# Kernel tuning notes

Measured on AMD Instinct MI355X. Metric: run time of the kernel, lower is better.

The kernel has to match this reference:

```python
import jax, jax.numpy as jnp
import numpy as np

B, U, NBS, S = 128, 4, 64, 408
EM_WEIGHT = 0.01  # config['loss']['em_property_weight']


def setup_inputs() -> dict:
    key = jax.random.key(0)
    ks = jax.random.split(key, 11)
    return {
        "atten_re": jax.random.normal(ks[0], (B, U, S), jnp.float32),
        "atten_im": jax.random.normal(ks[1], (B, U, S), jnp.float32),
        "rad_re": jax.random.normal(ks[2], (B, U, NBS, S), jnp.float32),
        "rad_im": jax.random.normal(ks[3], (B, U, NBS, S), jnp.float32),
        "tgt_re": jax.random.normal(ks[4], (B, U, NBS, S), jnp.float32),
        "tgt_im": jax.random.normal(ks[5], (B, U, NBS, S), jnp.float32),
        "weights": jax.random.uniform(ks[6], (S,), jnp.float32),
        "positions": jax.random.normal(ks[7], (B, 3), jnp.float32),
        "ue_positions": jax.random.normal(ks[8], (B, 3), jnp.float32),
        "view_directions": jax.random.normal(ks[9], (B, 3), jnp.float32),
        "bs_antenna_ids": jax.random.randint(ks[10], (B,), 0, NBS, jnp.int64),
    }


def reference(atten_re, atten_im, rad_re, rad_im, tgt_re, tgt_im, weights,
              positions, ue_positions, view_directions, bs_antenna_ids):
    # Vectorized form of the triple loop: the ray-tracer stub contributes
    # nothing; accumulated signal = attenuation * radiation (complex mul),
    # with attenuation broadcast over the BS-antenna axis.
    ar = atten_re[:, :, None, :]  # [B,U,1,S]
    ai = atten_im[:, :, None, :]
    pred_re = ar * rad_re - ai * rad_im  # [B,U,NBS,S]
    pred_im = ar * rad_im + ai * rad_re
    # MSE on real + imag parts, weighted per subcarrier, summed.
    se = (pred_re - tgt_re) ** 2 + (pred_im - tgt_im) ** 2
    received_loss = jnp.sum(se * weights[None, None, None, :])
    # EM property regularization (torch.abs on complex -> magnitude).
    atten_mag = jnp.sqrt(atten_re ** 2 + atten_im ** 2)
    rad_mag = jnp.sqrt(rad_re ** 2 + rad_im ** 2)
    em_loss = (jnp.mean(jax.nn.relu(atten_mag - 1.0) ** 2)
               + jnp.mean(jax.nn.relu(rad_mag - 10.0) ** 2))
    return received_loss + EM_WEIGHT * em_loss
```

## Files before the change

### kernel.cpp

```cpp
#include <hip/hip_runtime.h>

constexpr int kB   = 128;
constexpr int kU   = 4;
constexpr int kNBS = 64;
constexpr int kS   = 408;
constexpr int kS4  = kS / 4;
constexpr unsigned kNQ = (unsigned)kB * kU * kNBS * kS4;
constexpr unsigned kThreads = kNQ / 4;
constexpr unsigned kRowStep = 8192;
constexpr float kEmW     = 0.01f;
constexpr float kInvNRad = 1.0f / ((float)kB * kU * kNBS * kS);
constexpr float kInvNAtt = 1.0f / ((float)kB * kU * kS);

typedef float vfloat4 __attribute__((ext_vector_type(4)));

__global__ void __launch_bounds__(256)
prism_loss_kernel(const vfloat4* __restrict__ atten_re,
                  const vfloat4* __restrict__ atten_im,
                  const vfloat4* __restrict__ rad_re,
                  const vfloat4* __restrict__ rad_im,
                  const vfloat4* __restrict__ tgt_re,
                  const vfloat4* __restrict__ tgt_im,
                  const vfloat4* __restrict__ weights,
                  float* __restrict__ out)
{
    const unsigned tid  = blockIdx.x * 256 + threadIdx.x;
    const unsigned row0 = tid / 102u;
    const unsigned s4   = tid - row0 * 102u;
    const unsigned abase = (row0 >> 6) * 102u + s4;
    const bool do_att = ((row0 & 63u) == 0u);

    const vfloat4 w = weights[s4];

    vfloat4 ar[4], ai[4], rr[4], ri[4], tr[4], ti[4];
    #pragma unroll
    for (int i = 0; i < 4; ++i) {
        const unsigned q = tid + (unsigned)i * kThreads;
        const unsigned a = abase + (unsigned)i * (kRowStep / kNBS) * 102u;
        ar[i] = atten_re[a];
        ai[i] = atten_im[a];
        rr[i] = __builtin_nontemporal_load(&rad_re[q]);
        ri[i] = __builtin_nontemporal_load(&rad_im[q]);
        tr[i] = __builtin_nontemporal_load(&tgt_re[q]);
        ti[i] = __builtin_nontemporal_load(&tgt_im[q]);
    }

    float recv   = 0.0f;
    float em_rad = 0.0f;
    float em_att = 0.0f;

    #pragma unroll
    for (int i = 0; i < 4; ++i) {
        #pragma unroll
        for (int c = 0; c < 4; ++c) {
            const float a_r = ar[i][c], a_i = ai[i][c];
            const float r_r = rr[i][c], r_i = ri[i][c];
            const float pr = a_r * r_r - a_i * r_i;
            const float pi = a_r * r_i + a_i * r_r;
            const float dr = pr - tr[i][c];
            const float di = pi - ti[i][c];
            recv = fmaf((dr * dr + di * di), w[c], recv);
            float rm = sqrtf(fmaf(r_r, r_r, r_i * r_i)) - 10.0f;
            rm = fmaxf(rm, 0.0f);
            em_rad = fmaf(rm, rm, em_rad);
            if (do_att) {
                float am = sqrtf(fmaf(a_r, a_r, a_i * a_i)) - 1.0f;
                am = fmaxf(am, 0.0f);
                em_att = fmaf(am, am, em_att);
            }
        }
    }

    float acc = recv + kEmW * (em_rad * kInvNRad + em_att * kInvNAtt);

    #pragma unroll
    for (int off = 32; off > 0; off >>= 1)
        acc += __shfl_down(acc, off, 64);

    __shared__ float sdata[4];
    const int lane = threadIdx.x & 63;
    const int wave = threadIdx.x >> 6;
    if (lane == 0) sdata[wave] = acc;
    __syncthreads();
    if (threadIdx.x == 0) {
        atomicAdd(out, sdata[0] + sdata[1] + sdata[2] + sdata[3]);
    }
}

extern "C" void kernel_launch(void* const* d_in, const int* in_sizes, int n_in,
                              void* d_out, int out_size, void* d_ws, size_t ws_size,
                              hipStream_t stream) {
    const vfloat4* atten_re = (const vfloat4*)d_in[0];
    const vfloat4* atten_im = (const vfloat4*)d_in[1];
    const vfloat4* rad_re   = (const vfloat4*)d_in[2];
    const vfloat4* rad_im   = (const vfloat4*)d_in[3];
    const vfloat4* tgt_re   = (const vfloat4*)d_in[4];
    const vfloat4* tgt_im   = (const vfloat4*)d_in[5];
    const vfloat4* weights  = (const vfloat4*)d_in[6];
    float* out = (float*)d_out;

    (void)hipMemsetAsync(out, 0, sizeof(float), stream);

    prism_loss_kernel<<<(int)(kThreads / 256), 256, 0, stream>>>(
        atten_re, atten_im, rad_re, rad_im, tgt_re, tgt_im, weights, out);
}
```

Before: 223.7 us.

## Process eight antenna rows per thread sharing one attenuation load

After: 210.7 us. -5.8%, faster.

```diff
diff --git a/kernel.cpp b/kernel.cpp
--- a/kernel.cpp
+++ b/kernel.cpp
@@ -6,8 +6,8 @@
 constexpr int kS   = 408;
 constexpr int kS4  = kS / 4;
 constexpr unsigned kNQ = (unsigned)kB * kU * kNBS * kS4;
-constexpr unsigned kThreads = kNQ / 4;
-constexpr unsigned kRowStep = 8192;
+constexpr int kChunk   = 8;
+constexpr unsigned kThreads = kNQ / kChunk;
 constexpr float kEmW     = 0.01f;
 constexpr float kInvNRad = 1.0f / ((float)kB * kU * kNBS * kS);
 constexpr float kInvNAtt = 1.0f / ((float)kB * kU * kS);
@@ -24,50 +24,58 @@
                   const vfloat4* __restrict__ weights,
                   float* __restrict__ out)
 {
-    const unsigned tid  = blockIdx.x * 256 + threadIdx.x;
-    const unsigned row0 = tid / 102u;
-    const unsigned s4   = tid - row0 * 102u;
-    const unsigned abase = (row0 >> 6) * 102u + s4;
-    const bool do_att = ((row0 & 63u) == 0u);
+    const unsigned tid   = blockIdx.x * 256 + threadIdx.x;
+    const unsigned rem   = tid / 102u;
+    const unsigned s4    = tid - rem * 102u;
+    const unsigned chunk = rem & 7u;
+    const unsigned bu    = rem >> 3;
+    const unsigned qbase = (bu * 64u + chunk * 8u) * 102u + s4;
+    const unsigned abase = bu * 102u + s4;
+    const bool do_att = (chunk == 0u);
 
-    const vfloat4 w = weights[s4];
-
-    vfloat4 ar[4], ai[4], rr[4], ri[4], tr[4], ti[4];
-    #pragma unroll
-    for (int i = 0; i < 4; ++i) {
-        const unsigned q = tid + (unsigned)i * kThreads;
-        const unsigned a = abase + (unsigned)i * (kRowStep / kNBS) * 102u;
-        ar[i] = atten_re[a];
-        ai[i] = atten_im[a];
-        rr[i] = __builtin_nontemporal_load(&rad_re[q]);
-        ri[i] = __builtin_nontemporal_load(&rad_im[q]);
-        tr[i] = __builtin_nontemporal_load(&tgt_re[q]);
-        ti[i] = __builtin_nontemporal_load(&tgt_im[q]);
-    }
+    const vfloat4 w  = weights[s4];
+    const vfloat4 ar = atten_re[abase];
+    const vfloat4 ai = atten_im[abase];
 
     float recv   = 0.0f;
     float em_rad = 0.0f;
     float em_att = 0.0f;
 
     #pragma unroll
-    for (int i = 0; i < 4; ++i) {
+    for (int half = 0; half < 2; ++half) {
+        vfloat4 rr[4], ri[4], tr[4], ti[4];
+        #pragma unroll
+        for (int j = 0; j < 4; ++j) {
+            const unsigned q = qbase + (unsigned)(half * 4 + j) * 102u;
+            rr[j] = __builtin_nontemporal_load(&rad_re[q]);
+            ri[j] = __builtin_nontemporal_load(&rad_im[q]);
+            tr[j] = __builtin_nontemporal_load(&tgt_re[q]);
+            ti[j] = __builtin_nontemporal_load(&tgt_im[q]);
+        }
+        #pragma unroll
+        for (int j = 0; j < 4; ++j) {
+            #pragma unroll
+            for (int c = 0; c < 4; ++c) {
+                const float a_r = ar[c], a_i = ai[c];
+                const float r_r = rr[j][c], r_i = ri[j][c];
+                const float pr = a_r * r_r - a_i * r_i;
+                const float pi = a_r * r_i + a_i * r_r;
+                const float dr = pr - tr[j][c];
+                const float di = pi - ti[j][c];
+                recv = fmaf((dr * dr + di * di), w[c], recv);
+                float rm = sqrtf(fmaf(r_r, r_r, r_i * r_i)) - 10.0f;
+                rm = fmaxf(rm, 0.0f);
+                em_rad = fmaf(rm, rm, em_rad);
+            }
+        }
+    }
+
+    if (do_att) {
         #pragma unroll
         for (int c = 0; c < 4; ++c) {
-            const float a_r = ar[i][c], a_i = ai[i][c];
-            const float r_r = rr[i][c], r_i = ri[i][c];
-            const float pr = a_r * r_r - a_i * r_i;
-            const float pi = a_r * r_i + a_i * r_r;
-            const float dr = pr - tr[i][c];
-            const float di = pi - ti[i][c];
-            recv = fmaf((dr * dr + di * di), w[c], recv);
-            float rm = sqrtf(fmaf(r_r, r_r, r_i * r_i)) - 10.0f;
-            rm = fmaxf(rm, 0.0f);
-            em_rad = fmaf(rm, rm, em_rad);
-            if (do_att) {
-                float am = sqrtf(fmaf(a_r, a_r, a_i * a_i)) - 1.0f;
-                am = fmaxf(am, 0.0f);
-                em_att = fmaf(am, am, em_att);
-            }
+            float am = sqrtf(fmaf(ar[c], ar[c], ai[c] * ai[c])) - 1.0f;
+            am = fmaxf(am, 0.0f);
+            em_att = fmaf(am, am, em_att);
         }
     }
 
```
